# Optimization experiments

Hardware: AMD Instinct MI355X
Metric: run time of the kernel (lower is better)

## Reference

```python
import jax, jax.numpy as jnp
import numpy as np

ALPHA = 0.2  # LeakyReLU negative slope
NEG_INF = -1e9


def setup_inputs() -> dict:
    key = jax.random.key(0)
    k1, k2, k3, k4 = jax.random.split(key, 4)
    B, N, Fin, Fout = 8, 2048, 128, 64
    h = jax.random.normal(k1, (B, N, Fin), dtype=jnp.float32)
    adj_mask = jax.random.randint(k2, (B, N, N), 0, 2).astype(jnp.int32)
    # xavier_uniform-style scales
    W = jax.random.uniform(k3, (Fout, Fin), dtype=jnp.float32,
                           minval=-1.0, maxval=1.0) * np.sqrt(6.0 / (Fin + Fout))
    a = jax.random.uniform(k4, (2 * Fout,), dtype=jnp.float32,
                           minval=-1.0, maxval=1.0) * np.sqrt(6.0 / (2 * Fout + 1))
    return {"h": h, "adj_mask": adj_mask, "W": W, "a": a}


def reference(h, adj_mask, W, a):
    # Wh: [B, N, Fout]
    Wh = jnp.einsum("bnf,of->bno", h, W)
    Fout = Wh.shape[-1]
    a1, a2 = a[:Fout], a[Fout:]
    # additive decomposition of a([Wh_i || Wh_j]): e_ij = leakyrelu(s1_i + s2_j)
    s1 = Wh @ a1  # [B, N]
    s2 = Wh @ a2  # [B, N]
    e = jax.nn.leaky_relu(s1[:, :, None] + s2[:, None, :], negative_slope=ALPHA)  # [B,N,N]
    e = jnp.where(adj_mask == 0, NEG_INF, e)
    attention = jax.nn.softmax(e, axis=-1)
    # dropout is identity in eval mode / p effectively 0 for the reference
    h_prime = jnp.einsum("bij,bjo->bio", attention, Wh)
    return h_prime
```

## Files before the change

kernel.cpp:

```cpp
#include <hip/hip_runtime.h>
#include <hip/hip_fp16.h>
#include <math.h>

#define LRELU_ALPHA 0.2f
#define NEG_INF -1000000000.0f
#define L2E 1.44269504088896340736f

constexpr int B_ = 8, N_ = 2048, FIN = 128, FOUT = 64;

typedef _Float16 __attribute__((ext_vector_type(8))) f16x8;
typedef float __attribute__((ext_vector_type(4))) f32x4;

__device__ __forceinline__ void gload16(const void* g, void* l) {
  __builtin_amdgcn_global_load_lds(
      (const __attribute__((address_space(1))) void*)g,
      (__attribute__((address_space(3))) void*)l, 16, 0, 0);
}

__global__ __launch_bounds__(256) void k_wh(
    const float* __restrict__ h, const float* __restrict__ W,
    const float* __restrict__ a, unsigned short* __restrict__ WhT,
    float* __restrict__ s1, float* __restrict__ s2) {
  __shared__ float Wt[128][65];
  __shared__ float hs[16][128];

  const int t = threadIdx.x;
  const int row0 = blockIdx.x * 16;

  for (int e = t; e < 64 * 128; e += 256) {
    int o = e >> 7, f = e & 127;
    Wt[f][o] = W[e];
  }
  {
    const float4* hg = (const float4*)(h + (size_t)row0 * FIN);
    for (int i4 = t; i4 < 16 * 32; i4 += 256) {
      int r = i4 >> 5, f4 = i4 & 31;
      *(float4*)&hs[r][f4 * 4] = hg[i4];
    }
  }
  __syncthreads();

  const int wave = t >> 6, lane = t & 63;
  float acc[4] = {0.f, 0.f, 0.f, 0.f};
#pragma unroll 4
  for (int f4 = 0; f4 < 32; ++f4) {
    float w0 = Wt[4 * f4 + 0][lane], w1 = Wt[4 * f4 + 1][lane];
    float w2 = Wt[4 * f4 + 2][lane], w3 = Wt[4 * f4 + 3][lane];
#pragma unroll
    for (int r = 0; r < 4; ++r) {
      float4 hv = *(const float4*)&hs[wave * 4 + r][f4 * 4];
      acc[r] += hv.x * w0 + hv.y * w1 + hv.z * w2 + hv.w * w3;
    }
  }

  const float a1v = a[lane], a2v = a[64 + lane];
  const int b = row0 / N_;
#pragma unroll
  for (int r = 0; r < 4; ++r) {
    const int row = row0 + wave * 4 + r;
    const int n = row - b * N_;
    const float v = acc[r];
    WhT[((size_t)b * 64 + lane) * N_ + n] = __half_as_ushort(__float2half(v));
    float p1 = v * a1v, p2 = v * a2v;
#pragma unroll
    for (int d = 32; d; d >>= 1) {
      p1 += __shfl_xor(p1, d, 64);
      p2 += __shfl_xor(p2, d, 64);
    }
    if (lane == 0) { s1[row] = p1; s2[row] = p2; }
  }
}

__global__ __launch_bounds__(256, 4) void k_attn(
    const unsigned short* __restrict__ WhT,
    const float* __restrict__ s1g, const float* __restrict__ s2g,
    const int* __restrict__ adj, float* __restrict__ out) {
  __shared__ __align__(16) unsigned char sbuf[2][16 * 1024];
  __shared__ float s2s[N_];

  const int t = threadIdx.x;
  const int wave = t >> 6, lane = t & 63;
  const int m = lane & 15, q = lane >> 4;
  const int b = blockIdx.x;
  const int i0 = blockIdx.y * 16;
  const int jw = wave * 512;

  {
    const float4* s2R = (const float4*)(s2g + (size_t)b * N_);
    for (int i = t; i < N_ / 4; i += 256) {
      float4 v = s2R[i];
      v.x *= L2E; v.y *= L2E; v.z *= L2E; v.w *= L2E;
      ((float4*)s2s)[i] = v;
    }
  }

  const float s1r = s1g[b * N_ + i0 + m];
  const float c1 = (s1r - 2.0f) * L2E;
  const float c2 = (LRELU_ALPHA * s1r - 2.0f) * L2E;

  f16x8 ones;
#pragma unroll
  for (int j = 0; j < 8; ++j) ones[j] = (_Float16)1.0f;

  const int* adjR =
      adj + (size_t)b * N_ * N_ + (size_t)(i0 + m) * N_ + jw + q * 8;
  const unsigned short* whL =
      WhT + (size_t)b * 64 * N_ + (size_t)m * N_ + jw + q * 8;

  unsigned char* d0 = sbuf[0] + wave * 4096;
  unsigned char* d1 = sbuf[1] + wave * 4096;

#define STAGE(D, c)                                                       \
  {                                                                       \
    _Pragma("unroll") for (int g = 0; g < 4; ++g)                         \
        gload16(whL + (size_t)g * 16 * N_ + (c) * 32, (D) + g * 1024);    \
  }
#define ISSUE(R0, R1, c)                                 \
  {                                                      \
    const int4* ap = (const int4*)(adjR + (c) * 32);     \
    R0 = ap[0];                                          \
    R1 = ap[1];                                          \
  }
#define CONSUME(R0, R1, D, c)                                                \
  {                                                                          \
    const float* sp = &s2s[jw + (c) * 32 + q * 8];                           \
    float4 sv0 = *(const float4*)sp;                                         \
    float4 sv1 = *(const float4*)(sp + 4);                                   \
    float xs[8] = {sv0.x, sv0.y, sv0.z, sv0.w, sv1.x, sv1.y, sv1.z, sv1.w};  \
    int avs[8] = {R0.x, R0.y, R0.z, R0.w, R1.x, R1.y, R1.z, R1.w};           \
    f16x8 af;                                                                \
    _Pragma("unroll") for (int j = 0; j < 8; ++j) {                          \
      float x = xs[j];                                                       \
      float e = fmaxf(c1 + x, fmaf(LRELU_ALPHA, x, c2));                     \
      e = avs[j] ? e : NEG_INF;                                              \
      af[j] = (_Float16)__builtin_amdgcn_exp2f(e);  \
    }                                                                        \
    f16x8 bf0 = *(const f16x8*)((D) + 0 * 1024 + lane * 16);                 \
    f16x8 bf1 = *(const f16x8*)((D) + 1 * 1024 + lane * 16);                 \
    f16x8 bf2 = *(const f16x8*)((D) + 2 * 1024 + lane * 16);                 \
    f16x8 bf3 = *(const f16x8*)((D) + 3 * 1024 + lane * 16);                 \
    acc0 = __builtin_amdgcn_mfma_f32_16x16x32_f16(af, bf0, acc0, 0, 0, 0);   \
    acc1 = __builtin_amdgcn_mfma_f32_16x16x32_f16(af, bf1, acc1, 0, 0, 0);   \
    acc2 = __builtin_amdgcn_mfma_f32_16x16x32_f16(af, bf2, acc2, 0, 0, 0);   \
    acc3 = __builtin_amdgcn_mfma_f32_16x16x32_f16(af, bf3, acc3, 0, 0, 0);   \
    accS = __builtin_amdgcn_mfma_f32_16x16x32_f16(af, ones, accS, 0, 0, 0);  \
  }
#define FV(NN) asm volatile("s_waitcnt vmcnt(" #NN ")" ::: "memory");
#define FL() asm volatile("s_waitcnt lgkmcnt(0)" ::: "memory");

  int4 rA0, rA1, rB0, rB1;
  f32x4 acc0 = {0.f, 0.f, 0.f, 0.f}, acc1 = acc0, acc2 = acc0, acc3 = acc0,
        accS = acc0;

  __syncthreads();

  ISSUE(rA0, rA1, 0) STAGE(d0, 0)
  ISSUE(rB0, rB1, 1) STAGE(d1, 1)

  for (int c = 0; c < 14; c += 2) {
    FV(6) CONSUME(rA0, rA1, d0, c)
    FL() ISSUE(rA0, rA1, c + 2) STAGE(d0, c + 2)
    FV(6) CONSUME(rB0, rB1, d1, c + 1)
    FL() ISSUE(rB0, rB1, c + 3) STAGE(d1, c + 3)
  }
  FV(6) CONSUME(rA0, rA1, d0, 14)
  FV(0) CONSUME(rB0, rB1, d1, 15)

  {
    float* redw = (float*)d0;
#pragma unroll
    for (int r = 0; r < 4; ++r) {
      redw[(q * 4 + r) * 64 + 0 * 16 + m] = acc0[r];
      redw[(q * 4 + r) * 64 + 1 * 16 + m] = acc1[r];
      redw[(q * 4 + r) * 64 + 2 * 16 + m] = acc2[r];
      redw[(q * 4 + r) * 64 + 3 * 16 + m] = acc3[r];
    }
    if (m == 0) {
      float* redSw = (float*)d1;
#pragma unroll
      for (int r = 0; r < 4; ++r) redSw[q * 4 + r] = accS[r];
    }
  }
  __syncthreads();

  {
    const int row = t >> 4, c4 = t & 15;
    float4 v = {0.f, 0.f, 0.f, 0.f};
    float l = 0.f;
#pragma unroll
    for (int w2 = 0; w2 < 4; ++w2) {
      float4 pv = ((const float4*)(sbuf[0] + w2 * 4096))[row * 16 + c4];
      v.x += pv.x; v.y += pv.y; v.z += pv.z; v.w += pv.w;
      l += ((const float*)(sbuf[1] + w2 * 4096))[row];
    }
    const float inv = (l == 0.f) ? 1.f : 1.f / l;
    float4 o;
    o.x = v.x * inv; o.y = v.y * inv; o.z = v.z * inv; o.w = v.w * inv;
    ((float4*)(out + ((size_t)b * N_ + i0 + row) * FOUT))[c4] = o;
  }
#undef STAGE
#undef ISSUE
#undef CONSUME
#undef FV
#undef FL
}

extern "C" void kernel_launch(void* const* d_in, const int* in_sizes, int n_in,
                              void* d_out, int out_size, void* d_ws, size_t ws_size,
                              hipStream_t stream) {
  const float* h   = (const float*)d_in[0];
  const int*   adj = (const int*)d_in[1];
  const float* W   = (const float*)d_in[2];
  const float* a   = (const float*)d_in[3];
  float* out = (float*)d_out;

  unsigned short* WhT = (unsigned short*)d_ws;
  float* s1 = (float*)(WhT + (size_t)B_ * 64 * N_);
  float* s2 = s1 + (size_t)B_ * N_;

  k_wh<<<dim3(B_ * N_ / 16), 256, 0, stream>>>(h, W, a, WhT, s1, s2);
  k_attn<<<dim3(B_, N_ / 16), 256, 0, stream>>>(WhT, s1, s2, adj, out);
}
```

Baseline: 237.0 us.

## Pre-pack adjacency mask into bitmasks via ballot before attention kernel

Adds a streaming kernel that reads the int32 adjacency matrix once and turns it into 64-bit ballot bitmasks (one bit per edge). The attention kernel then loads each row's mask bits up front instead of streaming int4 adjacency loads inside its pipelined loop. This frees vector-memory slots and registers in the MFMA loop and simplifies its wait counts. In exchange it adds an extra launch plus a small bitmask write and read-back, while the full adjacency read still happens in the pack kernel.

```diff
diff --git a/kernel.cpp b/kernel.cpp
--- a/kernel.cpp
+++ b/kernel.cpp
@@ -71,10 +71,30 @@
   }
 }
 
+__global__ __launch_bounds__(256) void k_pack(
+    const int* __restrict__ adj, unsigned long long* __restrict__ pk) {
+  const int wave = threadIdx.x >> 6, lane = threadIdx.x & 63;
+  const size_t row = (size_t)blockIdx.x * 4 + wave;
+  const int4* src = (const int4*)(adj + row * 2048);
+  unsigned long long* dst = pk + row * 32;
+#pragma unroll
+  for (int k = 0; k < 8; ++k) {
+    int4 v = src[k * 64 + lane];
+    unsigned long long b0 = __ballot(v.x != 0);
+    unsigned long long b1 = __ballot(v.y != 0);
+    unsigned long long b2 = __ballot(v.z != 0);
+    unsigned long long b3 = __ballot(v.w != 0);
+    unsigned long long sel = (lane == 0) ? b0
+                           : (lane == 1) ? b1
+                           : (lane == 2) ? b2 : b3;
+    if (lane < 4) dst[k * 4 + lane] = sel;
+  }
+}
+
 __global__ __launch_bounds__(256, 4) void k_attn(
     const unsigned short* __restrict__ WhT,
     const float* __restrict__ s1g, const float* __restrict__ s2g,
-    const int* __restrict__ adj, float* __restrict__ out) {
+    const unsigned long long* __restrict__ pk, float* __restrict__ out) {
   __shared__ __align__(16) unsigned char sbuf[2][16 * 1024];
   __shared__ float s2s[N_];
 
@@ -102,37 +122,45 @@
 #pragma unroll
   for (int j = 0; j < 8; ++j) ones[j] = (_Float16)1.0f;
 
-  const int* adjR =
-      adj + (size_t)b * N_ * N_ + (size_t)(i0 + m) * N_ + jw + q * 8;
   const unsigned short* whL =
       WhT + (size_t)b * 64 * N_ + (size_t)m * N_ + jw + q * 8;
 
   unsigned char* d0 = sbuf[0] + wave * 4096;
   unsigned char* d1 = sbuf[1] + wave * 4096;
+
+  __syncthreads();
+
+  const unsigned long long* pkL =
+      pk + (size_t)(b * N_ + i0 + m) * 32 + wave * 8;
+  ulonglong2 mA01 = *(const ulonglong2*)(pkL + 0);
+  ulonglong2 mA23 = *(const ulonglong2*)(pkL + 2);
+  ulonglong2 mB01 = *(const ulonglong2*)(pkL + 4);
+  ulonglong2 mB23 = *(const ulonglong2*)(pkL + 6);
 
 #define STAGE(D, c)                                                       \
   {                                                                       \
     _Pragma("unroll") for (int g = 0; g < 4; ++g)                         \
         gload16(whL + (size_t)g * 16 * N_ + (c) * 32, (D) + g * 1024);    \
   }
-#define ISSUE(R0, R1, c)                                 \
-  {                                                      \
-    const int4* ap = (const int4*)(adjR + (c) * 32);     \
-    R0 = ap[0];                                          \
-    R1 = ap[1];                                          \
-  }
-#define CONSUME(R0, R1, D, c)                                                \
+#define CONSUME(M0, M1, M2, M3, D, c)                                        \
   {                                                                          \
+    const unsigned l0 = ((unsigned)(c)&7u) * 8u + (unsigned)q * 2u;          \
+    const unsigned w0 = (unsigned)((M0) >> l0);                              \
+    const unsigned w1 = (unsigned)((M1) >> l0);                              \
+    const unsigned w2 = (unsigned)((M2) >> l0);                              \
+    const unsigned w3 = (unsigned)((M3) >> l0);                              \
     const float* sp = &s2s[jw + (c) * 32 + q * 8];                           \
     float4 sv0 = *(const float4*)sp;                                         \
     float4 sv1 = *(const float4*)(sp + 4);                                   \
     float xs[8] = {sv0.x, sv0.y, sv0.z, sv0.w, sv1.x, sv1.y, sv1.z, sv1.w};  \
-    int avs[8] = {R0.x, R0.y, R0.z, R0.w, R1.x, R1.y, R1.z, R1.w};           \
     f16x8 af;                                                                \
     _Pragma("unroll") for (int j = 0; j < 8; ++j) {                          \
       float x = xs[j];                                                       \
       float e = fmaxf(c1 + x, fmaf(LRELU_ALPHA, x, c2));                     \
-      e = avs[j] ? e : NEG_INF;                                              \
+      const unsigned sel = ((j & 3) == 0) ? w0                               \
+                         : ((j & 3) == 1) ? w1                               \
+                         : ((j & 3) == 2) ? w2 : w3;                         \
+      e = ((sel >> (j >> 2)) & 1u) ? e : NEG_INF;                            \
       af[j] = (_Float16)__builtin_amdgcn_exp2f(e);  \
     }                                                                        \
     f16x8 bf0 = *(const f16x8*)((D) + 0 * 1024 + lane * 16);                 \
@@ -146,25 +174,23 @@
     accS = __builtin_amdgcn_mfma_f32_16x16x32_f16(af, ones, accS, 0, 0, 0);  \
   }
 #define FV(NN) asm volatile("s_waitcnt vmcnt(" #NN ")" ::: "memory");
-#define FL() asm volatile("s_waitcnt lgkmcnt(0)" ::: "memory");
-
-  int4 rA0, rA1, rB0, rB1;
+
   f32x4 acc0 = {0.f, 0.f, 0.f, 0.f}, acc1 = acc0, acc2 = acc0, acc3 = acc0,
         accS = acc0;
 
-  __syncthreads();
-
-  ISSUE(rA0, rA1, 0) STAGE(d0, 0)
-  ISSUE(rB0, rB1, 1) STAGE(d1, 1)
-
-  for (int c = 0; c < 14; c += 2) {
-    FV(6) CONSUME(rA0, rA1, d0, c)
-    FL() ISSUE(rA0, rA1, c + 2) STAGE(d0, c + 2)
-    FV(6) CONSUME(rB0, rB1, d1, c + 1)
-    FL() ISSUE(rB0, rB1, c + 3) STAGE(d1, c + 3)
-  }
-  FV(6) CONSUME(rA0, rA1, d0, 14)
-  FV(0) CONSUME(rB0, rB1, d1, 15)
+  STAGE(d0, 0)
+  STAGE(d1, 1)
+
+  for (int c = 0; c < 8; c += 2) {
+    FV(4) CONSUME(mA01.x, mA01.y, mA23.x, mA23.y, d0, c) STAGE(d0, c + 2)
+    FV(4) CONSUME(mA01.x, mA01.y, mA23.x, mA23.y, d1, c + 1) STAGE(d1, c + 3)
+  }
+  for (int c = 8; c < 14; c += 2) {
+    FV(4) CONSUME(mB01.x, mB01.y, mB23.x, mB23.y, d0, c) STAGE(d0, c + 2)
+    FV(4) CONSUME(mB01.x, mB01.y, mB23.x, mB23.y, d1, c + 1) STAGE(d1, c + 3)
+  }
+  FV(4) CONSUME(mB01.x, mB01.y, mB23.x, mB23.y, d0, 14)
+  FV(0) CONSUME(mB01.x, mB01.y, mB23.x, mB23.y, d1, 15)
 
   {
     float* redw = (float*)d0;
@@ -199,10 +225,8 @@
     ((float4*)(out + ((size_t)b * N_ + i0 + row) * FOUT))[c4] = o;
   }
 #undef STAGE
-#undef ISSUE
 #undef CONSUME
 #undef FV
-#undef FL
 }
 
 extern "C" void kernel_launch(void* const* d_in, const int* in_sizes, int n_in,
@@ -217,7 +241,9 @@
   unsigned short* WhT = (unsigned short*)d_ws;
   float* s1 = (float*)(WhT + (size_t)B_ * 64 * N_);
   float* s2 = s1 + (size_t)B_ * N_;
-
+  unsigned long long* pkw = (unsigned long long*)(s2 + (size_t)B_ * N_);
+
+  k_pack<<<dim3(B_ * N_ / 4), 256, 0, stream>>>(adj, pkw);
   k_wh<<<dim3(B_ * N_ / 16), 256, 0, stream>>>(h, W, a, WhT, s1, s2);
-  k_attn<<<dim3(B_, N_ / 16), 256, 0, stream>>>(WhT, s1, s2, adj, out);
-}
+  k_attn<<<dim3(B_, N_ / 16), 256, 0, stream>>>(WhT, s1, s2, pkw, out);
+}
```

Measured after the change: 245.6 us. 1.04x slower.
